# Kernel optimization log

Measured on AMD Instinct MI355X. Metric: run time of the kernel, lower is better.

Reference implementation:

```python
import jax, jax.numpy as jnp
import numpy as np

Z_RES, N_RES = 128, 512
M_PTS = 2_000_000


def trilinear_devoxelize(grid, coords):
    """Gather-based trilinear interpolation.
    grid:   (Z, N, N, C) voxel grid
    coords: (M, 3) float positions in voxel index space (z, x, y)
    returns (M, C)
    """
    Zd, Nd = grid.shape[0], grid.shape[1]
    c0f = jnp.floor(coords)
    frac = coords - c0f                      # (M, 3) fractional offsets
    maxi = jnp.array([Zd - 1, Nd - 1, Nd - 1], dtype=jnp.int32)
    c0 = jnp.clip(c0f.astype(jnp.int32), 0, maxi)
    c1 = jnp.clip(c0 + 1, 0, maxi)
    fz, fx, fy = frac[:, 0:1], frac[:, 1:2], frac[:, 2:3]
    gz, gx, gy = 1.0 - fz, 1.0 - fx, 1.0 - fy

    def g(zi, xi, yi):
        return grid[zi, xi, yi]              # (M, C) gather

    out = (g(c0[:, 0], c0[:, 1], c0[:, 2]) * gz * gx * gy
         + g(c0[:, 0], c0[:, 1], c1[:, 2]) * gz * gx * fy
         + g(c0[:, 0], c1[:, 1], c0[:, 2]) * gz * fx * gy
         + g(c0[:, 0], c1[:, 1], c1[:, 2]) * gz * fx * fy
         + g(c1[:, 0], c0[:, 1], c0[:, 2]) * fz * gx * gy
         + g(c1[:, 0], c0[:, 1], c1[:, 2]) * fz * gx * fy
         + g(c1[:, 0], c1[:, 1], c0[:, 2]) * fz * fx * gy
         + g(c1[:, 0], c1[:, 1], c1[:, 2]) * fz * fx * fy)
    return out


def setup_inputs() -> dict:
    key = jax.random.key(0)
    k1, k2 = jax.random.split(key)
    extents = jnp.array([Z_RES - 1, N_RES - 1, N_RES - 1], jnp.float32)
    coords = jax.random.uniform(k1, (M_PTS, 3), dtype=jnp.float32) * extents
    # init_scale = 1.0 -> albedo ~ U[0,1); normal initialized to zeros (per module)
    albedo = jax.random.uniform(k2, (Z_RES, N_RES, N_RES), dtype=jnp.float32)
    normal = jnp.zeros((Z_RES, N_RES, N_RES, 3), dtype=jnp.float32)
    return {"coords": coords, "albedo": albedo, "normal": normal}


def reference(coords, albedo, normal):
    base_normal = jnp.array([-1.0, 0.0, 0.0], dtype=jnp.float32)
    a = trilinear_devoxelize(albedo[..., None], coords)[:, 0]   # (M,)
    n = trilinear_devoxelize(normal, coords)                    # (M, 3)
    a = jax.nn.elu(a)
    n = jnp.tanh(n) + base_normal
    # F.normalize(dim=1, eps=1e-12): divide by max(||n||, eps)
    norm = jnp.maximum(jnp.linalg.norm(n, axis=1, keepdims=True), 1e-12)
    n = n / norm
    return (a, n)
```

## Files before the change

### kernel.cpp

```cpp
#include <hip/hip_runtime.h>
#include <math.h>

#define ZR 128
#define NR 512

__global__ __launch_bounds__(256) void devox_kernel(
    const float* __restrict__ coords,
    const float* __restrict__ albedo,
    const float* __restrict__ normal,
    float* __restrict__ out_a,
    float* __restrict__ out_n,
    int M)
{
    int i = blockIdx.x * blockDim.x + threadIdx.x;
    if (i >= M) return;

    float cz = coords[3 * i + 0];
    float cx = coords[3 * i + 1];
    float cy = coords[3 * i + 2];

    float fz0 = floorf(cz), fx0 = floorf(cx), fy0 = floorf(cy);
    float fz = cz - fz0, fx = cx - fx0, fy = cy - fy0;

    int z0 = min(max((int)fz0, 0), ZR - 1);
    int x0 = min(max((int)fx0, 0), NR - 1);
    int y0 = min(max((int)fy0, 0), NR - 1);
    int z1 = min(z0 + 1, ZR - 1);
    int x1 = min(x0 + 1, NR - 1);
    int y1 = min(y0 + 1, NR - 1);

    float gz = 1.0f - fz, gx = 1.0f - fx, gy = 1.0f - fy;

    float w000 = gz * gx * gy, w001 = gz * gx * fy;
    float w010 = gz * fx * gy, w011 = gz * fx * fy;
    float w100 = fz * gx * gy, w101 = fz * gx * fy;
    float w110 = fz * fx * gy, w111 = fz * fx * fy;

    size_t b00 = ((size_t)z0 * NR + x0) * NR;
    size_t b01 = ((size_t)z0 * NR + x1) * NR;
    size_t b10 = ((size_t)z1 * NR + x0) * NR;
    size_t b11 = ((size_t)z1 * NR + x1) * NR;

    float a =
        albedo[b00 + y0] * w000 + albedo[b00 + y1] * w001 +
        albedo[b01 + y0] * w010 + albedo[b01 + y1] * w011 +
        albedo[b10 + y0] * w100 + albedo[b10 + y1] * w101 +
        albedo[b11 + y0] * w110 + albedo[b11 + y1] * w111;

    float n0 = 0.0f, n1 = 0.0f, n2 = 0.0f;
#define ACC(base, yy, w)                                        \
    {                                                           \
        const float* p = normal + ((base) + (size_t)(yy)) * 3;  \
        n0 += p[0] * (w);                                       \
        n1 += p[1] * (w);                                       \
        n2 += p[2] * (w);                                       \
    }
    ACC(b00, y0, w000); ACC(b00, y1, w001);
    ACC(b01, y0, w010); ACC(b01, y1, w011);
    ACC(b10, y0, w100); ACC(b10, y1, w101);
    ACC(b11, y0, w110); ACC(b11, y1, w111);
#undef ACC

    a = (a > 0.0f) ? a : expm1f(a);

    n0 = tanhf(n0) - 1.0f;
    n1 = tanhf(n1);
    n2 = tanhf(n2);

    float nrm = sqrtf(n0 * n0 + n1 * n1 + n2 * n2);
    nrm = fmaxf(nrm, 1e-12f);
    float inv = 1.0f / nrm;

    out_a[i] = a;
    out_n[3 * i + 0] = n0 * inv;
    out_n[3 * i + 1] = n1 * inv;
    out_n[3 * i + 2] = n2 * inv;
}

extern "C" void kernel_launch(void* const* d_in, const int* in_sizes, int n_in,
                              void* d_out, int out_size, void* d_ws, size_t ws_size,
                              hipStream_t stream) {
    const float* coords = (const float*)d_in[0];
    const float* albedo = (const float*)d_in[1];
    const float* normal = (const float*)d_in[2];

    int M = in_sizes[0] / 3;
    float* out = (float*)d_out;
    float* out_a = out;
    float* out_n = out + M;

    int block = 256;
    int grid = (M + block - 1) / block;
    devox_kernel<<<grid, block, 0, stream>>>(coords, albedo, normal, out_a, out_n, M);
}
```

Measured before the change: 825.5 us.

## Bucket-sort points by spatial cell before trilinear gather

```diff
diff --git a/kernel.cpp b/kernel.cpp
--- a/kernel.cpp
+++ b/kernel.cpp
@@ -3,8 +3,152 @@
 
 #define ZR 128
 #define NR 512
-
-__global__ __launch_bounds__(256) void devox_kernel(
+#define NBUCKETS 4096
+
+__device__ __forceinline__ int bucket_of(float cz, float cx, float cy) {
+    int z0 = min(max((int)floorf(cz), 0), ZR - 1);
+    int x0 = min(max((int)floorf(cx), 0), NR - 1);
+    int y0 = min(max((int)floorf(cy), 0), NR - 1);
+    return ((z0 >> 3) << 8) | ((x0 >> 5) << 4) | (y0 >> 5);
+}
+
+__global__ __launch_bounds__(256) void hist_kernel(
+    const float* __restrict__ coords, unsigned int* __restrict__ hist, int M)
+{
+    __shared__ unsigned int h[NBUCKETS];
+    for (int k = threadIdx.x; k < NBUCKETS; k += 256) h[k] = 0;
+    __syncthreads();
+
+    int stride = gridDim.x * 256;
+    for (int i = blockIdx.x * 256 + threadIdx.x; i < M; i += stride) {
+        float cz = coords[3 * i + 0];
+        float cx = coords[3 * i + 1];
+        float cy = coords[3 * i + 2];
+        atomicAdd(&h[bucket_of(cz, cx, cy)], 1u);
+    }
+    __syncthreads();
+    for (int k = threadIdx.x; k < NBUCKETS; k += 256) {
+        unsigned int v = h[k];
+        if (v) atomicAdd(&hist[k], v);
+    }
+}
+
+__global__ __launch_bounds__(256) void scan_kernel(unsigned int* __restrict__ hist)
+{
+    __shared__ unsigned int partial[256];
+    int tid = threadIdx.x;
+    unsigned int vals[NBUCKETS / 256];
+    unsigned int s = 0;
+#pragma unroll
+    for (int k = 0; k < NBUCKETS / 256; k++) {
+        vals[k] = hist[tid * (NBUCKETS / 256) + k];
+        s += vals[k];
+    }
+    partial[tid] = s;
+    __syncthreads();
+    for (int off = 1; off < 256; off <<= 1) {
+        unsigned int v = (tid >= off) ? partial[tid - off] : 0u;
+        __syncthreads();
+        partial[tid] += v;
+        __syncthreads();
+    }
+    unsigned int run = (tid == 0) ? 0u : partial[tid - 1];
+#pragma unroll
+    for (int k = 0; k < NBUCKETS / 256; k++) {
+        unsigned int c = vals[k];
+        hist[tid * (NBUCKETS / 256) + k] = run;
+        run += c;
+    }
+}
+
+__global__ __launch_bounds__(256) void scatter_kernel(
+    const float* __restrict__ coords, unsigned int* __restrict__ cursor,
+    float4* __restrict__ sorted, int M)
+{
+    int i = blockIdx.x * 256 + threadIdx.x;
+    if (i >= M) return;
+    float cz = coords[3 * i + 0];
+    float cx = coords[3 * i + 1];
+    float cy = coords[3 * i + 2];
+    int b = bucket_of(cz, cx, cy);
+    unsigned int pos = atomicAdd(&cursor[b], 1u);
+    sorted[pos] = make_float4(cz, cx, cy, __int_as_float(i));
+}
+
+__global__ __launch_bounds__(256) void interp_kernel(
+    const float4* __restrict__ sorted,
+    const float* __restrict__ albedo,
+    const float* __restrict__ normal,
+    float* __restrict__ out_a,
+    float* __restrict__ out_n,
+    int M)
+{
+    int j = blockIdx.x * 256 + threadIdx.x;
+    if (j >= M) return;
+
+    float4 p = sorted[j];
+    float cz = p.x, cx = p.y, cy = p.z;
+    int idx = __float_as_int(p.w);
+
+    float fz0 = floorf(cz), fx0 = floorf(cx), fy0 = floorf(cy);
+    float fz = cz - fz0, fx = cx - fx0, fy = cy - fy0;
+
+    int z0 = min(max((int)fz0, 0), ZR - 1);
+    int x0 = min(max((int)fx0, 0), NR - 1);
+    int y0 = min(max((int)fy0, 0), NR - 1);
+    int z1 = min(z0 + 1, ZR - 1);
+    int x1 = min(x0 + 1, NR - 1);
+    int y1 = min(y0 + 1, NR - 1);
+
+    float gz = 1.0f - fz, gx = 1.0f - fx, gy = 1.0f - fy;
+
+    float w000 = gz * gx * gy, w001 = gz * gx * fy;
+    float w010 = gz * fx * gy, w011 = gz * fx * fy;
+    float w100 = fz * gx * gy, w101 = fz * gx * fy;
+    float w110 = fz * fx * gy, w111 = fz * fx * fy;
+
+    size_t b00 = ((size_t)z0 * NR + x0) * NR;
+    size_t b01 = ((size_t)z0 * NR + x1) * NR;
+    size_t b10 = ((size_t)z1 * NR + x0) * NR;
+    size_t b11 = ((size_t)z1 * NR + x1) * NR;
+
+    float a =
+        albedo[b00 + y0] * w000 + albedo[b00 + y1] * w001 +
+        albedo[b01 + y0] * w010 + albedo[b01 + y1] * w011 +
+        albedo[b10 + y0] * w100 + albedo[b10 + y1] * w101 +
+        albedo[b11 + y0] * w110 + albedo[b11 + y1] * w111;
+
+    float n0 = 0.0f, n1 = 0.0f, n2 = 0.0f;
+#define ACC(base, yy, w)                                        \
+    {                                                           \
+        const float* q = normal + ((base) + (size_t)(yy)) * 3;  \
+        n0 += q[0] * (w);                                       \
+        n1 += q[1] * (w);                                       \
+        n2 += q[2] * (w);                                       \
+    }
+    ACC(b00, y0, w000); ACC(b00, y1, w001);
+    ACC(b01, y0, w010); ACC(b01, y1, w011);
+    ACC(b10, y0, w100); ACC(b10, y1, w101);
+    ACC(b11, y0, w110); ACC(b11, y1, w111);
+#undef ACC
+
+    a = (a > 0.0f) ? a : expm1f(a);
+
+    n0 = tanhf(n0) - 1.0f;
+    n1 = tanhf(n1);
+    n2 = tanhf(n2);
+
+    float nrm = sqrtf(n0 * n0 + n1 * n1 + n2 * n2);
+    nrm = fmaxf(nrm, 1e-12f);
+    float inv = 1.0f / nrm;
+
+    out_a[idx] = a;
+    out_n[3 * idx + 0] = n0 * inv;
+    out_n[3 * idx + 1] = n1 * inv;
+    out_n[3 * idx + 2] = n2 * inv;
+}
+
+__global__ __launch_bounds__(256) void devox_direct(
     const float* __restrict__ coords,
     const float* __restrict__ albedo,
     const float* __restrict__ normal,
@@ -12,7 +156,7 @@
     float* __restrict__ out_n,
     int M)
 {
-    int i = blockIdx.x * blockDim.x + threadIdx.x;
+    int i = blockIdx.x * 256 + threadIdx.x;
     if (i >= M) return;
 
     float cz = coords[3 * i + 0];
@@ -30,7 +174,6 @@
     int y1 = min(y0 + 1, NR - 1);
 
     float gz = 1.0f - fz, gx = 1.0f - fx, gy = 1.0f - fy;
-
     float w000 = gz * gx * gy, w001 = gz * gx * fy;
     float w010 = gz * fx * gy, w011 = gz * fx * fy;
     float w100 = fz * gx * gy, w101 = fz * gx * fy;
@@ -50,10 +193,10 @@
     float n0 = 0.0f, n1 = 0.0f, n2 = 0.0f;
 #define ACC(base, yy, w)                                        \
     {                                                           \
-        const float* p = normal + ((base) + (size_t)(yy)) * 3;  \
-        n0 += p[0] * (w);                                       \
-        n1 += p[1] * (w);                                       \
-        n2 += p[2] * (w);                                       \
+        const float* q = normal + ((base) + (size_t)(yy)) * 3;  \
+        n0 += q[0] * (w);                                       \
+        n1 += q[1] * (w);                                       \
+        n2 += q[2] * (w);                                       \
     }
     ACC(b00, y0, w000); ACC(b00, y1, w001);
     ACC(b01, y0, w010); ACC(b01, y1, w011);
@@ -62,11 +205,9 @@
 #undef ACC
 
     a = (a > 0.0f) ? a : expm1f(a);
-
     n0 = tanhf(n0) - 1.0f;
     n1 = tanhf(n1);
     n2 = tanhf(n2);
-
     float nrm = sqrtf(n0 * n0 + n1 * n1 + n2 * n2);
     nrm = fmaxf(nrm, 1e-12f);
     float inv = 1.0f / nrm;
@@ -89,7 +230,23 @@
     float* out_a = out;
     float* out_n = out + M;
 
-    int block = 256;
-    int grid = (M + block - 1) / block;
-    devox_kernel<<<grid, block, 0, stream>>>(coords, albedo, normal, out_a, out_n, M);
-}
+    int nblk = (M + 255) / 256;
+
+    size_t hist_bytes = (size_t)NBUCKETS * 4;
+    size_t sorted_off = (hist_bytes + 255) & ~(size_t)255;
+    size_t needed = sorted_off + (size_t)M * 16;
+
+    if (ws_size < needed) {
+        devox_direct<<<nblk, 256, 0, stream>>>(coords, albedo, normal, out_a, out_n, M);
+        return;
+    }
+
+    unsigned int* hist = (unsigned int*)d_ws;
+    float4* sorted = (float4*)((char*)d_ws + sorted_off);
+
+    hipMemsetAsync(hist, 0, hist_bytes, stream);
+    hist_kernel<<<256, 256, 0, stream>>>(coords, hist, M);
+    scan_kernel<<<1, 256, 0, stream>>>(hist);
+    scatter_kernel<<<nblk, 256, 0, stream>>>(coords, hist, sorted, M);
+    interp_kernel<<<nblk, 256, 0, stream>>>(sorted, albedo, normal, out_a, out_n, M);
+}
```

Result: slower. 902.0 us (+9.3%).
